# Kernel optimization log

Hardware: AMD Instinct MI355X
Metric: run time of the kernel (lower is better)

Reference implementation:

```python
import jax, jax.numpy as jnp
import numpy as np

S, B, K = 1024, 16, 1024
QD, KD = 1024, 1024


def setup_inputs() -> dict:
    key = jax.random.key(0)
    k1, k2, k3, k4 = jax.random.split(key, 4)
    queries = jax.random.normal(k1, (S, B, QD), dtype=jnp.float32)
    keys = jax.random.normal(k2, (B, K, KD), dtype=jnp.float32)
    null_mask = jax.random.randint(k3, (B, K), 0, 2).astype(jnp.bool_)
    W_in = jax.random.normal(k4, (KD, QD), dtype=jnp.float32) * 0.02
    return {"queries": queries, "keys": keys, "null_mask": null_mask, "W_in": W_in}


def reference(queries, keys, null_mask, W_in):
    # queries: (S, B, QD); keys: (B, K, KD); null_mask: (B, K); W_in: (KD, QD)
    t_query = jnp.einsum('sbq,dq->sbd', queries, W_in)          # linear_in, no bias
    alpha = jnp.einsum('sbd,bkd->sbk', t_query, keys)           # unscaled bilinear scores
    alpha = jnp.where(null_mask[None, :, :], -jnp.inf, alpha)   # masked_fill_
    att_weight = jax.nn.softmax(alpha, axis=2)                  # (S, B, K)
    attened_keys = jnp.einsum('sbk,bkd->sbd', att_weight, keys) # (S, B, KD)
    return (attened_keys, alpha)
```

## Files before the change

kernel.cpp:

```cpp
#include <hip/hip_runtime.h>
#include <math.h>

#define S_DIM 1024
#define B_DIM 16
#define K_DIM 1024
#define QD_DIM 1024
#define KD_DIM 1024
#define MASK_NEG (-3.0e38f)

using short8v = __attribute__((ext_vector_type(8))) short;
using float4v = __attribute__((ext_vector_type(4))) float;
using uint4v  = __attribute__((ext_vector_type(4))) uint;

#define MFMA(a, b, c) __builtin_amdgcn_mfma_f32_16x16x32_bf16(a, b, c, 0, 0, 0)
#define BAR()   __builtin_amdgcn_s_barrier()
#define SB0()   __builtin_amdgcn_sched_barrier(0)
#define PRIO(x) __builtin_amdgcn_s_setprio(x)
#define VMCNT(N) asm volatile("s_waitcnt vmcnt(" #N ")" ::: "memory")
#define LGKM0()  asm volatile("s_waitcnt lgkmcnt(0)" ::: "memory")


__device__ __forceinline__ void gll16(const void* g, void* l) {
    __builtin_amdgcn_global_load_lds((const __attribute__((address_space(1))) unsigned int*)g,
                                     (__attribute__((address_space(3))) unsigned int*)l,
                                     16, 0, 0);
}

__device__ __forceinline__ void split4(const float4 v, uint2& hi, uint2& lo) {
    uint ax = __float_as_uint(v.x), ay = __float_as_uint(v.y);
    uint az = __float_as_uint(v.z), aw = __float_as_uint(v.w);
    hi.x = __builtin_amdgcn_perm(ay, ax, 0x07060302u);
    hi.y = __builtin_amdgcn_perm(aw, az, 0x07060302u);
    float rx = v.x - __uint_as_float(ax & 0xFFFF0000u);
    float ry = v.y - __uint_as_float(ay & 0xFFFF0000u);
    float rz = v.z - __uint_as_float(az & 0xFFFF0000u);
    float rw = v.w - __uint_as_float(aw & 0xFFFF0000u);
    lo.x = __builtin_amdgcn_perm(__float_as_uint(ry), __float_as_uint(rx), 0x07060302u);
    lo.y = __builtin_amdgcn_perm(__float_as_uint(rw), __float_as_uint(rz), 0x07060302u);
}

__device__ __forceinline__ int twiddle(int l) {
    int b0 = (l ^ (l >> 2) ^ (l >> 4)) & 1;
    int b1 = ((l >> 1) ^ (l >> 3)) & 1;
    int b2 = ((l >> 2) ^ (l >> 4)) & 1;
    return (l & 0x38) | (b2 << 2) | (b1 << 1) | b0;
}
__device__ __forceinline__ int fragoff(int R, int quad) {
    return (((R << 2) | quad) ^ (R & 7)) << 3;
}

struct Ctx {
    int w, quad, l15, wm, wn, srow, scol;
    int arow, ac, ws0, ws1;
    int offA[4], offB[8];
};

__device__ __forceinline__ Ctx make_ctx(int t) {
    Ctx c;
    const int lane = t & 63;
    c.w = t >> 6; c.quad = lane >> 4; c.l15 = lane & 15;
    c.wm = c.w >> 1; c.wn = c.w & 1;
    const int sl = twiddle(lane);
    c.srow = c.w * 32 + (sl >> 2);
    c.scol = (sl & 3) * 8;
    c.arow = t >> 1; c.ac = t & 1;
    const int c0 = c.ac * 2;
    c.ws0 = ((c.arow << 2) | c0) ^ (c.arow & 7);
    c.ws1 = ((c.arow << 2) | (c0 + 1)) ^ (c.arow & 7);
    #pragma unroll
    for (int mt = 0; mt < 4; ++mt) { int R = c.wm * 64 + mt * 16 + c.l15; c.offA[mt] = fragoff(R, c.quad); }
    #pragma unroll
    for (int nt = 0; nt < 8; ++nt) { int R = c.wn * 128 + nt * 16 + c.l15; c.offB[nt] = fragoff(R, c.quad); }
    return c;
}

__device__ __forceinline__ void stage2(const short* __restrict__ plane, int row0, int k0,
                                       short* tile, const Ctx& c) {
    const short* g0 = plane + (size_t)(row0 + c.srow) * 1024 + k0 + c.scol;
    gll16(g0, tile + c.w * 1024);
    gll16(g0 + (size_t)16 * 1024, tile + c.w * 1024 + 512);
}

__device__ __forceinline__ void mfma8x4(const short8v (&a)[4], const short8v (&bb)[8],
                                        float4v (&acc)[4][8]) {
    #pragma unroll
    for (int nt = 0; nt < 8; ++nt)
        #pragma unroll
        for (int mt = 0; mt < 4; ++mt)
            acc[mt][nt] = MFMA(a[mt], bb[nt], acc[mt][nt]);
}

__device__ __forceinline__ void load4(const float4* __restrict__ P, int kn, float4 (&v)[4]) {
    #pragma unroll
    for (int i = 0; i < 4; ++i) v[i] = P[kn / 4 + i];
}

__device__ __forceinline__ void write_split(const float4 (&va)[4], short* N0, short* N1,
                                            int ws0, int ws1) {
    uint2 h[4], l[4];
    #pragma unroll
    for (int i = 0; i < 4; ++i) split4(va[i], h[i], l[i]);
    uint4v v0, v1;
    v0[0] = h[0].x; v0[1] = h[0].y; v0[2] = h[1].x; v0[3] = h[1].y;
    v1[0] = h[2].x; v1[1] = h[2].y; v1[2] = h[3].x; v1[3] = h[3].y;
    *(uint4v*)(N0 + ws0 * 8) = v0;
    *(uint4v*)(N0 + ws1 * 8) = v1;
    v0[0] = l[0].x; v0[1] = l[0].y; v0[2] = l[1].x; v0[3] = l[1].y;
    v1[0] = l[2].x; v1[1] = l[2].y; v1[2] = l[3].x; v1[3] = l[3].y;
    *(uint4v*)(N1 + ws0 * 8) = v0;
    *(uint4v*)(N1 + ws1 * 8) = v1;
}

__device__ __forceinline__ void writeA_exp(const float4 (&va)[4], float Mv, float Lv,
                                           short* N0, short* N1, int ws0, int ws1) {
    float4 p[4];
    #pragma unroll
    for (int i = 0; i < 4; ++i) {
        p[i].x = __expf(va[i].x - Mv) * Lv;
        p[i].y = __expf(va[i].y - Mv) * Lv;
        p[i].z = __expf(va[i].z - Mv) * Lv;
        p[i].w = __expf(va[i].w - Mv) * Lv;
    }
    write_split(p, N0, N1, ws0, ws1);
}

__device__ __forceinline__ void loadT(const float* __restrict__ fB, int kn, float4 (&f)[4]) {
    #pragma unroll
    for (int i = 0; i < 4; ++i) f[i] = *(const float4*)(fB + (size_t)(kn + i) * 1024);
}
__device__ __forceinline__ void writeT(const float4 (&f)[4], short* N2, short* N3,
                                       int kq, int dd) {
    #pragma unroll
    for (int e = 0; e < 4; ++e) {
        float4 g;
        g.x = (&f[0].x)[e]; g.y = (&f[1].x)[e];
        g.z = (&f[2].x)[e]; g.w = (&f[3].x)[e];
        uint2 h, l;
        split4(g, h, l);
        const int R = dd * 4 + e;
        const int byteoff = ((((R << 2) | (kq >> 1)) ^ (R & 7)) << 4) + (kq & 1) * 8;
        *(uint2*)((char*)N2 + byteoff) = h;
        *(uint2*)((char*)N3 + byteoff) = l;
    }
}

__global__ __launch_bounds__(256) void k_split(const float* __restrict__ src,
                                               short* __restrict__ h, short* __restrict__ l) {
    const size_t base = ((size_t)blockIdx.x * 256 + threadIdx.x) * 4;
    const float4 v = *(const float4*)(src + base);
    uint2 hh, ll;
    split4(v, hh, ll);
    *(uint2*)(h + base) = hh;
    *(uint2*)(l + base) = ll;
}

__global__ __launch_bounds__(256) void k_stats(const float* __restrict__ alpha,
                                               float* __restrict__ mx,
                                               float* __restrict__ il) {
    const int r = blockIdx.x;
    const int t = threadIdx.x;
    const float4 v = ((const float4*)(alpha + (size_t)r * K_DIM))[t];
    float m = fmaxf(fmaxf(v.x, v.y), fmaxf(v.z, v.w));
    #pragma unroll
    for (int o = 1; o < 64; o <<= 1) m = fmaxf(m, __shfl_xor(m, o, 64));
    __shared__ float redm[4];
    __shared__ float reds[4];
    const int wid = t >> 6;
    if ((t & 63) == 0) redm[wid] = m;
    __syncthreads();
    const float M = fmaxf(fmaxf(redm[0], redm[1]), fmaxf(redm[2], redm[3]));
    float s = expf(v.x - M) + expf(v.y - M) + expf(v.z - M) + expf(v.w - M);
    #pragma unroll
    for (int o = 1; o < 64; o <<= 1) s += __shfl_xor(s, o, 64);
    if ((t & 63) == 0) reds[wid] = s;
    __syncthreads();
    if (t == 0) {
        mx[r] = M;
        il[r] = 1.0f / (reds[0] + reds[1] + reds[2] + reds[3]);
    }
}

template<bool DS>
__device__ __forceinline__ void step_g1(const float4* __restrict__ qP, int kn,
                                        const short* __restrict__ Wh, const short* __restrict__ Wl, int n0,
                                        const short* C0, const short* C1, const short* C2, const short* C3,
                                        short* N0, short* N1, short* N2, short* N3,
                                        const Ctx& c, float4v (&acc)[4][8]) {
    short8v ah[4], bh[8];
    #pragma unroll
    for (int mt = 0; mt < 4; ++mt) ah[mt] = *(const short8v*)(C0 + c.offA[mt]);
    #pragma unroll
    for (int nt = 0; nt < 8; ++nt) bh[nt] = *(const short8v*)(C2 + c.offB[nt]);
    float4 qv[4];
    if (DS) { load4(qP, kn, qv); SB0(); stage2(Wh, n0, kn, N2, c); }
    SB0(); BAR(); LGKM0(); SB0();
    PRIO(1); mfma8x4(ah, bh, acc); PRIO(0); SB0(); BAR();

    short8v al[4];
    #pragma unroll
    for (int mt = 0; mt < 4; ++mt) al[mt] = *(const short8v*)(C1 + c.offA[mt]);
    if (DS) { stage2(Wl, n0, kn, N3, c); }
    SB0(); BAR(); LGKM0(); SB0();
    PRIO(1); mfma8x4(al, bh, acc); PRIO(0); SB0(); BAR();

    if (DS) { VMCNT(4); } else { VMCNT(0); }
    SB0(); BAR();
    short8v bl[8];
    #pragma unroll
    for (int nt = 0; nt < 8; ++nt) bl[nt] = *(const short8v*)(C3 + c.offB[nt]);
    LGKM0(); SB0();
    PRIO(1); mfma8x4(ah, bl, acc); PRIO(0);
    if (DS) {
        write_split(qv, N0, N1, c.ws0, c.ws1);
        LGKM0();
        VMCNT(2);
    }
    SB0(); BAR();
}

__global__ __launch_bounds__(512, 2) void g1k(const float* __restrict__ Q,
                                              const short* __restrict__ Wh, const short* __restrict__ Wl,
                                              short* __restrict__ TQh, short* __restrict__ TQl) {
    __shared__ __align__(16) short lds[65536];
    const int t = threadIdx.x;
    const int m0 = blockIdx.y * 256, n0 = blockIdx.x * 256;
    const Ctx c = make_ctx(t);
    const float4* qP = (const float4*)(Q + (size_t)(m0 + c.arow) * QD_DIM + c.ac * 16);
    short *T00 = lds,         *T01 = lds + 8192,  *T02 = lds + 16384, *T03 = lds + 24576;
    short *T10 = lds + 32768, *T11 = lds + 40960, *T12 = lds + 49152, *T13 = lds + 57344;

    float4v acc[4][8] = {};
    {
        float4 qv[4];
        load4(qP, 0, qv); SB0();
        stage2(Wh, n0, 0, T02, c);
        stage2(Wl, n0, 0, T03, c);
        VMCNT(4); SB0();
        write_split(qv, T00, T01, c.ws0, c.ws1);
        LGKM0();
        VMCNT(2); SB0();
        BAR();
    }
    #pragma unroll 1
    for (int it = 0; it < 15; ++it) {
        step_g1<true>(qP, (2 * it + 1) * 32, Wh, Wl, n0, T00, T01, T02, T03, T10, T11, T12, T13, c, acc);
        step_g1<true>(qP, (2 * it + 2) * 32, Wh, Wl, n0, T10, T11, T12, T13, T00, T01, T02, T03, c, acc);
    }
    step_g1<true >(qP, 31 * 32, Wh, Wl, n0, T00, T01, T02, T03, T10, T11, T12, T13, c, acc);
    step_g1<false>(qP, 0,       Wh, Wl, n0, T10, T11, T12, T13, T00, T01, T02, T03, c, acc);

    #pragma unroll
    for (int mt = 0; mt < 4; ++mt)
        #pragma unroll
        for (int reg = 0; reg < 4; ++reg) {
            const int m = m0 + c.wm * 64 + mt * 16 + c.quad * 4 + reg;
            const int s = m >> 4, bq = m & 15;
            short* th = TQh + (size_t)bq * 1048576 + (size_t)s * 1024;
            short* tl = TQl + (size_t)bq * 1048576 + (size_t)s * 1024;
            #pragma unroll
            for (int nt = 0; nt < 8; ++nt) {
                const int n = n0 + c.wn * 128 + nt * 16 + c.l15;
                const float x = acc[mt][nt][reg];
                const uint u = __float_as_uint(x);
                th[n] = (short)(u >> 16);
                const float r2 = x - __uint_as_float(u & 0xFFFF0000u);
                tl[n] = (short)(__float_as_uint(r2) >> 16);
            }
        }
}

template<bool DS>
__device__ __forceinline__ void step_g2(const float4* __restrict__ kP, int kn,
                                        const short* __restrict__ Ahp, const short* __restrict__ Alp, int m0,
                                        const short* C0, const short* C1, const short* C2, const short* C3,
                                        short* N0, short* N1, short* N2, short* N3,
                                        const Ctx& c, float4v (&acc)[4][8]) {
    short8v ah[4], bh[8];
    #pragma unroll
    for (int mt = 0; mt < 4; ++mt) ah[mt] = *(const short8v*)(C0 + c.offA[mt]);
    #pragma unroll
    for (int nt = 0; nt < 8; ++nt) bh[nt] = *(const short8v*)(C2 + c.offB[nt]);
    float4 kv[4];
    if (DS) { load4(kP, kn, kv); SB0(); stage2(Ahp, m0, kn, N0, c); VMCNT(6); }
    else    { VMCNT(0); }
    SB0(); BAR(); LGKM0(); SB0();
    PRIO(1); mfma8x4(ah, bh, acc); PRIO(0); SB0(); BAR();

    short8v al[4];
    #pragma unroll
    for (int mt = 0; mt < 4; ++mt) al[mt] = *(const short8v*)(C1 + c.offA[mt]);
    if (DS) { stage2(Alp, m0, kn, N1, c); }
    SB0(); BAR(); LGKM0(); SB0();
    PRIO(1); mfma8x4(al, bh, acc); PRIO(0); SB0(); BAR();

    if (DS) { VMCNT(4); } else { VMCNT(0); }
    SB0(); BAR();
    short8v bl[8];
    #pragma unroll
    for (int nt = 0; nt < 8; ++nt) bl[nt] = *(const short8v*)(C3 + c.offB[nt]);
    LGKM0(); SB0();
    PRIO(1); mfma8x4(ah, bl, acc); PRIO(0);
    if (DS) {
        write_split(kv, N2, N3, c.ws0, c.ws1);
        LGKM0();
        VMCNT(2);
    }
    SB0(); BAR();
}

__global__ __launch_bounds__(512, 2) void g2k(const short* __restrict__ TQh, const short* __restrict__ TQl,
                                              const float* __restrict__ keys,
                                              const int* __restrict__ mask, float* __restrict__ alpha) {
    __shared__ __align__(16) short lds[65536];
    const int t = threadIdx.x;
    const int m0 = blockIdx.y * 256, n0 = blockIdx.x * 256, b = blockIdx.z;
    const Ctx c = make_ctx(t);
    const short* Ahp = TQh + (size_t)b * 1048576;
    const short* Alp = TQl + (size_t)b * 1048576;
    const float* Kb = keys + (size_t)b * K_DIM * KD_DIM;
    const float4* kP = (const float4*)(Kb + (size_t)(n0 + c.arow) * KD_DIM + c.ac * 16);
    short *T00 = lds,         *T01 = lds + 8192,  *T02 = lds + 16384, *T03 = lds + 24576;
    short *T10 = lds + 32768, *T11 = lds + 40960, *T12 = lds + 49152, *T13 = lds + 57344;

    float4v acc[4][8] = {};
    {
        float4 kv[4];
        load4(kP, 0, kv); SB0();
        stage2(Ahp, m0, 0, T00, c);
        VMCNT(2); SB0();
        write_split(kv, T02, T03, c.ws0, c.ws1);
        LGKM0(); SB0();
        stage2(Alp, m0, 0, T01, c);
        VMCNT(2); SB0();
        BAR();
    }
    #pragma unroll 1
    for (int it = 0; it < 15; ++it) {
        step_g2<true>(kP, (2 * it + 1) * 32, Ahp, Alp, m0, T00, T01, T02, T03, T10, T11, T12, T13, c, acc);
        step_g2<true>(kP, (2 * it + 2) * 32, Ahp, Alp, m0, T10, T11, T12, T13, T00, T01, T02, T03, c, acc);
    }
    step_g2<true >(kP, 31 * 32, Ahp, Alp, m0, T00, T01, T02, T03, T10, T11, T12, T13, c, acc);
    step_g2<false>(kP, 0,       Ahp, Alp, m0, T10, T11, T12, T13, T00, T01, T02, T03, c, acc);

    int mk[8];
    #pragma unroll
    for (int nt = 0; nt < 8; ++nt)
        mk[nt] = mask[b * K_DIM + n0 + c.wn * 128 + nt * 16 + c.l15];
    #pragma unroll
    for (int mt = 0; mt < 4; ++mt)
        #pragma unroll
        for (int reg = 0; reg < 4; ++reg) {
            const int m = m0 + c.wm * 64 + mt * 16 + c.quad * 4 + reg;
            #pragma unroll
            for (int nt = 0; nt < 8; ++nt) {
                const int n = n0 + c.wn * 128 + nt * 16 + c.l15;
                alpha[((size_t)m * B_DIM + b) * K_DIM + n] = mk[nt] ? MASK_NEG : acc[mt][nt][reg];
            }
        }
}

template<bool DS>
__device__ __forceinline__ void step_g3(const float4* __restrict__ aP, const float* __restrict__ fB, int kn,
                                        const short* C0, const short* C1, const short* C2, const short* C3,
                                        short* N0, short* N1, short* N2, short* N3,
                                        const Ctx& c, float Mv, float Lv, int kq, int dd,
                                        float4v (&acc)[4][8]) {
    short8v ah[4], bh[8];
    #pragma unroll
    for (int mt = 0; mt < 4; ++mt) ah[mt] = *(const short8v*)(C0 + c.offA[mt]);
    #pragma unroll
    for (int nt = 0; nt < 8; ++nt) bh[nt] = *(const short8v*)(C2 + c.offB[nt]);
    float4 av[4];
    if (DS) { load4(aP, kn, av); }
    SB0(); BAR(); LGKM0(); SB0();
    PRIO(1); mfma8x4(ah, bh, acc); PRIO(0); SB0(); BAR();

    short8v al[4];
    #pragma unroll
    for (int mt = 0; mt < 4; ++mt) al[mt] = *(const short8v*)(C1 + c.offA[mt]);
    float4 f[4];
    if (DS) { loadT(fB, kn, f); }
    SB0(); BAR(); LGKM0(); SB0();
    PRIO(1); mfma8x4(al, bh, acc); PRIO(0); SB0(); BAR();

    VMCNT(0);
    SB0(); BAR();
    short8v bl[8];
    #pragma unroll
    for (int nt = 0; nt < 8; ++nt) bl[nt] = *(const short8v*)(C3 + c.offB[nt]);
    LGKM0(); SB0();
    PRIO(1); mfma8x4(ah, bl, acc); PRIO(0);
    if (DS) {
        writeA_exp(av, Mv, Lv, N0, N1, c.ws0, c.ws1);
        writeT(f, N2, N3, kq, dd);
        LGKM0();
    }
    SB0(); BAR();
}

__global__ __launch_bounds__(512, 2) void g3k(const float* __restrict__ alpha,
                                              const float* __restrict__ keys,
                                              const float* __restrict__ mx, const float* __restrict__ il,
                                              float* __restrict__ outk) {
    __shared__ __align__(16) short lds[65536];
    const int t = threadIdx.x;
    const int m0 = blockIdx.y * 256, n0 = blockIdx.x * 256, b = blockIdx.z;
    const Ctx c = make_ctx(t);
    const float* Kb = keys + (size_t)b * K_DIM * KD_DIM;
    const float4* aP = (const float4*)(alpha + ((size_t)(m0 + c.arow) * B_DIM + b) * K_DIM + c.ac * 16);
    const float Mv = mx[(size_t)(m0 + c.arow) * B_DIM + b];
    const float Lv = il[(size_t)(m0 + c.arow) * B_DIM + b];
    const int kq = t & 7, dd = t >> 3;
    const float* fB = Kb + (size_t)(4 * kq) * KD_DIM + n0 + dd * 4;
    short *T00 = lds,         *T01 = lds + 8192,  *T02 = lds + 16384, *T03 = lds + 24576;
    short *T10 = lds + 32768, *T11 = lds + 40960, *T12 = lds + 49152, *T13 = lds + 57344;

    float4v acc[4][8] = {};
    {
        float4 av[4], f[4];
        load4(aP, 0, av); SB0();
        loadT(fB, 0, f);
        VMCNT(0); SB0();
        writeA_exp(av, Mv, Lv, T00, T01, c.ws0, c.ws1);
        writeT(f, T02, T03, kq, dd);
        LGKM0(); SB0();
        BAR();
    }
    #pragma unroll 1
    for (int it = 0; it < 15; ++it) {
        step_g3<true>(aP, fB, (2 * it + 1) * 32, T00, T01, T02, T03, T10, T11, T12, T13, c, Mv, Lv, kq, dd, acc);
        step_g3<true>(aP, fB, (2 * it + 2) * 32, T10, T11, T12, T13, T00, T01, T02, T03, c, Mv, Lv, kq, dd, acc);
    }
    step_g3<true >(aP, fB, 31 * 32, T00, T01, T02, T03, T10, T11, T12, T13, c, Mv, Lv, kq, dd, acc);
    step_g3<false>(aP, fB, 0,       T10, T11, T12, T13, T00, T01, T02, T03, c, Mv, Lv, kq, dd, acc);

    #pragma unroll
    for (int mt = 0; mt < 4; ++mt)
        #pragma unroll
        for (int reg = 0; reg < 4; ++reg) {
            const int m = m0 + c.wm * 64 + mt * 16 + c.quad * 4 + reg;
            #pragma unroll
            for (int nt = 0; nt < 8; ++nt) {
                const int n = n0 + c.wn * 128 + nt * 16 + c.l15;
                outk[((size_t)m * B_DIM + b) * KD_DIM + n] = acc[mt][nt][reg];
            }
        }
}

extern "C" void kernel_launch(void* const* d_in, const int* in_sizes, int n_in,
                              void* d_out, int out_size, void* d_ws, size_t ws_size,
                              hipStream_t stream) {
    const float* Q    = (const float*)d_in[0];
    const float* keys = (const float*)d_in[1];
    const int*   mask = (const int*)d_in[2];
    const float* W    = (const float*)d_in[3];

    float* out_att   = (float*)d_out;
    float* out_alpha = out_att + (size_t)S_DIM * B_DIM * KD_DIM;

    const size_t STREAM = (size_t)B_DIM * 1048576;

    short* TQh = (short*)d_ws;
    short* TQl = TQh + STREAM;
    float* mx  = (float*)((char*)d_ws + ((size_t)64 << 20));
    float* il  = mx + S_DIM * B_DIM;

    short* Wh = (short*)out_att;
    short* Wl = Wh + 1048576;

    dim3 blk(256), blkg(512);

    k_split<<<dim3(1024), blk, 0, stream>>>(W, Wh, Wl);

    g1k<<<dim3(KD_DIM / 256, (S_DIM * B_DIM) / 256), blkg, 0, stream>>>(Q, Wh, Wl, TQh, TQl);

    g2k<<<dim3(K_DIM / 256, S_DIM / 256, B_DIM), blkg, 0, stream>>>(TQh, TQl, keys, mask, out_alpha);

    k_stats<<<dim3(S_DIM * B_DIM), blk, 0, stream>>>(out_alpha, mx, il);

    g3k<<<dim3(KD_DIM / 256, S_DIM / 256, B_DIM), blkg, 0, stream>>>(out_alpha, keys, mx, il, out_att);
}
```

Measured before the change: 596.9 us.

## Pre-split keys into bf16 hi/lo and pre-transpose for GEMM staging

Adds a pass that splits keys into bf16 hi/lo halves once, so g2k can stage both operands with direct global-to-LDS loads instead of loading fp32 keys into registers and splitting them per tile. Adds a transpose-and-split kernel that writes keys^T as hi/lo into workspace, reusing the TQ buffer once g2k is done, so g3k also stages B via global-to-LDS and only converts the softmax A operand in registers. This removes repeated per-block conversion and the strided transpose loads in g3k. The cost is extra full passes over keys (split plus transpose) and scratch space borrowed from the output buffers.

Result: faster. 553.2 us (-7.3%).

```diff
diff --git a/kernel.cpp b/kernel.cpp
--- a/kernel.cpp
+++ b/kernel.cpp
@@ -124,26 +124,6 @@
     write_split(p, N0, N1, ws0, ws1);
 }
 
-__device__ __forceinline__ void loadT(const float* __restrict__ fB, int kn, float4 (&f)[4]) {
-    #pragma unroll
-    for (int i = 0; i < 4; ++i) f[i] = *(const float4*)(fB + (size_t)(kn + i) * 1024);
-}
-__device__ __forceinline__ void writeT(const float4 (&f)[4], short* N2, short* N3,
-                                       int kq, int dd) {
-    #pragma unroll
-    for (int e = 0; e < 4; ++e) {
-        float4 g;
-        g.x = (&f[0].x)[e]; g.y = (&f[1].x)[e];
-        g.z = (&f[2].x)[e]; g.w = (&f[3].x)[e];
-        uint2 h, l;
-        split4(g, h, l);
-        const int R = dd * 4 + e;
-        const int byteoff = ((((R << 2) | (kq >> 1)) ^ (R & 7)) << 4) + (kq & 1) * 8;
-        *(uint2*)((char*)N2 + byteoff) = h;
-        *(uint2*)((char*)N3 + byteoff) = l;
-    }
-}
-
 __global__ __launch_bounds__(256) void k_split(const float* __restrict__ src,
                                                short* __restrict__ h, short* __restrict__ l) {
     const size_t base = ((size_t)blockIdx.x * 256 + threadIdx.x) * 4;
@@ -152,6 +132,25 @@
     split4(v, hh, ll);
     *(uint2*)(h + base) = hh;
     *(uint2*)(l + base) = ll;
+}
+
+__global__ __launch_bounds__(256) void k_transpose(const float* __restrict__ keys,
+                                                   short* __restrict__ th, short* __restrict__ tl) {
+    __shared__ float T[32][33];
+    const int t = threadIdx.x;
+    const int b = blockIdx.z, d0 = blockIdx.x * 32, k0 = blockIdx.y * 32;
+    const float* Kb = keys + (size_t)b * K_DIM * KD_DIM;
+    const int ry = t >> 3, cx = (t & 7) * 4;
+    const float4 v = *(const float4*)(Kb + (size_t)(k0 + ry) * KD_DIM + d0 + cx);
+    T[ry][cx] = v.x; T[ry][cx + 1] = v.y; T[ry][cx + 2] = v.z; T[ry][cx + 3] = v.w;
+    __syncthreads();
+    float4 g;
+    g.x = T[cx][ry]; g.y = T[cx + 1][ry]; g.z = T[cx + 2][ry]; g.w = T[cx + 3][ry];
+    uint2 hh, ll;
+    split4(g, hh, ll);
+    const size_t o = (size_t)b * K_DIM * KD_DIM + (size_t)(d0 + ry) * K_DIM + k0 + cx;
+    *(uint2*)(th + o) = hh;
+    *(uint2*)(tl + o) = ll;
 }
 
 __global__ __launch_bounds__(256) void k_stats(const float* __restrict__ alpha,
@@ -270,8 +269,9 @@
 }
 
 template<bool DS>
-__device__ __forceinline__ void step_g2(const float4* __restrict__ kP, int kn,
-                                        const short* __restrict__ Ahp, const short* __restrict__ Alp, int m0,
+__device__ __forceinline__ void step_gg(const short* __restrict__ Ahp, const short* __restrict__ Alp,
+                                        const short* __restrict__ Bhp, const short* __restrict__ Blp,
+                                        int m0, int n0, int kn,
                                         const short* C0, const short* C1, const short* C2, const short* C3,
                                         short* N0, short* N1, short* N2, short* N3,
                                         const Ctx& c, float4v (&acc)[4][8]) {
@@ -280,8 +280,7 @@
     for (int mt = 0; mt < 4; ++mt) ah[mt] = *(const short8v*)(C0 + c.offA[mt]);
     #pragma unroll
     for (int nt = 0; nt < 8; ++nt) bh[nt] = *(const short8v*)(C2 + c.offB[nt]);
-    float4 kv[4];
-    if (DS) { load4(kP, kn, kv); SB0(); stage2(Ahp, m0, kn, N0, c); VMCNT(6); }
+    if (DS) { stage2(Ahp, m0, kn, N0, c); stage2(Bhp, n0, kn, N2, c); VMCNT(4); }
     else    { VMCNT(0); }
     SB0(); BAR(); LGKM0(); SB0();
     PRIO(1); mfma8x4(ah, bh, acc); PRIO(0); SB0(); BAR();
@@ -289,59 +288,45 @@
     short8v al[4];
     #pragma unroll
     for (int mt = 0; mt < 4; ++mt) al[mt] = *(const short8v*)(C1 + c.offA[mt]);
-    if (DS) { stage2(Alp, m0, kn, N1, c); }
+    if (DS) { stage2(Alp, m0, kn, N1, c); stage2(Blp, n0, kn, N3, c); }
     SB0(); BAR(); LGKM0(); SB0();
     PRIO(1); mfma8x4(al, bh, acc); PRIO(0); SB0(); BAR();
 
-    if (DS) { VMCNT(4); } else { VMCNT(0); }
-    SB0(); BAR();
     short8v bl[8];
     #pragma unroll
     for (int nt = 0; nt < 8; ++nt) bl[nt] = *(const short8v*)(C3 + c.offB[nt]);
-    LGKM0(); SB0();
-    PRIO(1); mfma8x4(ah, bl, acc); PRIO(0);
-    if (DS) {
-        write_split(kv, N2, N3, c.ws0, c.ws1);
-        LGKM0();
-        VMCNT(2);
-    }
-    SB0(); BAR();
+    if (DS) { VMCNT(4); }
+    SB0(); BAR(); LGKM0(); SB0();
+    PRIO(1); mfma8x4(ah, bl, acc); PRIO(0); SB0(); BAR();
+}
+
+__device__ __forceinline__ void core_gg(const short* __restrict__ Ahp, const short* __restrict__ Alp,
+                                        const short* __restrict__ Bhp, const short* __restrict__ Blp,
+                                        int m0, int n0, short* lds, const Ctx& c, float4v (&acc)[4][8]) {
+    short *T00 = lds,         *T01 = lds + 8192,  *T02 = lds + 16384, *T03 = lds + 24576;
+    short *T10 = lds + 32768, *T11 = lds + 40960, *T12 = lds + 49152, *T13 = lds + 57344;
+    stage2(Ahp, m0, 0, T00, c); stage2(Bhp, n0, 0, T02, c);
+    stage2(Alp, m0, 0, T01, c); stage2(Blp, n0, 0, T03, c);
+    VMCNT(4); SB0(); BAR();
+    #pragma unroll 1
+    for (int it = 0; it < 15; ++it) {
+        step_gg<true>(Ahp, Alp, Bhp, Blp, m0, n0, (2 * it + 1) * 32, T00, T01, T02, T03, T10, T11, T12, T13, c, acc);
+        step_gg<true>(Ahp, Alp, Bhp, Blp, m0, n0, (2 * it + 2) * 32, T10, T11, T12, T13, T00, T01, T02, T03, c, acc);
+    }
+    step_gg<true >(Ahp, Alp, Bhp, Blp, m0, n0, 31 * 32, T00, T01, T02, T03, T10, T11, T12, T13, c, acc);
+    step_gg<false>(Ahp, Alp, Bhp, Blp, m0, n0, 0,       T10, T11, T12, T13, T00, T01, T02, T03, c, acc);
 }
 
 __global__ __launch_bounds__(512, 2) void g2k(const short* __restrict__ TQh, const short* __restrict__ TQl,
-                                              const float* __restrict__ keys,
+                                              const short* __restrict__ Kh, const short* __restrict__ Kl,
                                               const int* __restrict__ mask, float* __restrict__ alpha) {
     __shared__ __align__(16) short lds[65536];
     const int t = threadIdx.x;
     const int m0 = blockIdx.y * 256, n0 = blockIdx.x * 256, b = blockIdx.z;
     const Ctx c = make_ctx(t);
-    const short* Ahp = TQh + (size_t)b * 1048576;
-    const short* Alp = TQl + (size_t)b * 1048576;
-    const float* Kb = keys + (size_t)b * K_DIM * KD_DIM;
-    const float4* kP = (const float4*)(Kb + (size_t)(n0 + c.arow) * KD_DIM + c.ac * 16);
-    short *T00 = lds,         *T01 = lds + 8192,  *T02 = lds + 16384, *T03 = lds + 24576;
-    short *T10 = lds + 32768, *T11 = lds + 40960, *T12 = lds + 49152, *T13 = lds + 57344;
-
     float4v acc[4][8] = {};
-    {
-        float4 kv[4];
-        load4(kP, 0, kv); SB0();
-        stage2(Ahp, m0, 0, T00, c);
-        VMCNT(2); SB0();
-        write_split(kv, T02, T03, c.ws0, c.ws1);
-        LGKM0(); SB0();
-        stage2(Alp, m0, 0, T01, c);
-        VMCNT(2); SB0();
-        BAR();
-    }
-    #pragma unroll 1
-    for (int it = 0; it < 15; ++it) {
-        step_g2<true>(kP, (2 * it + 1) * 32, Ahp, Alp, m0, T00, T01, T02, T03, T10, T11, T12, T13, c, acc);
-        step_g2<true>(kP, (2 * it + 2) * 32, Ahp, Alp, m0, T10, T11, T12, T13, T00, T01, T02, T03, c, acc);
-    }
-    step_g2<true >(kP, 31 * 32, Ahp, Alp, m0, T00, T01, T02, T03, T10, T11, T12, T13, c, acc);
-    step_g2<false>(kP, 0,       Ahp, Alp, m0, T10, T11, T12, T13, T00, T01, T02, T03, c, acc);
-
+    core_gg(TQh + (size_t)b * 1048576, TQl + (size_t)b * 1048576,
+            Kh + (size_t)b * 1048576, Kl + (size_t)b * 1048576, m0, n0, lds, c, acc);
     int mk[8];
     #pragma unroll
     for (int nt = 0; nt < 8; ++nt)
@@ -360,30 +345,35 @@
 }
 
 template<bool DS>
-__device__ __forceinline__ void step_g3(const float4* __restrict__ aP, const float* __restrict__ fB, int kn,
+__device__ __forceinline__ void step_g3(const float4* __restrict__ aP, int kn,
+                                        const short* __restrict__ Bhp, const short* __restrict__ Blp, int n0,
                                         const short* C0, const short* C1, const short* C2, const short* C3,
                                         short* N0, short* N1, short* N2, short* N3,
-                                        const Ctx& c, float Mv, float Lv, int kq, int dd,
+                                        const Ctx& c, float Mv, float Lv,
                                         float4v (&acc)[4][8]) {
     short8v ah[4], bh[8];
     #pragma unroll
     for (int mt = 0; mt < 4; ++mt) ah[mt] = *(const short8v*)(C0 + c.offA[mt]);
     #pragma unroll
     for (int nt = 0; nt < 8; ++nt) bh[nt] = *(const short8v*)(C2 + c.offB[nt]);
-    float4 av[4];
-    if (DS) { load4(aP, kn, av); }
+    float4 va[4];
+    if (DS) {
+        #pragma unroll
+        for (int i = 0; i < 4; ++i) va[i] = aP[kn / 4 + i];
+        stage2(Bhp, n0, kn, N2, c);
+    }
     SB0(); BAR(); LGKM0(); SB0();
     PRIO(1); mfma8x4(ah, bh, acc); PRIO(0); SB0(); BAR();
 
     short8v al[4];
     #pragma unroll
     for (int mt = 0; mt < 4; ++mt) al[mt] = *(const short8v*)(C1 + c.offA[mt]);
-    float4 f[4];
-    if (DS) { loadT(fB, kn, f); }
+    if (DS) { stage2(Blp, n0, kn, N3, c); }
     SB0(); BAR(); LGKM0(); SB0();
     PRIO(1); mfma8x4(al, bh, acc); PRIO(0); SB0(); BAR();
 
-    VMCNT(0);
+    if (DS) { VMCNT(4); }
+    else    { VMCNT(0); }
     SB0(); BAR();
     short8v bl[8];
     #pragma unroll
@@ -391,48 +381,49 @@
     LGKM0(); SB0();
     PRIO(1); mfma8x4(ah, bl, acc); PRIO(0);
     if (DS) {
-        writeA_exp(av, Mv, Lv, N0, N1, c.ws0, c.ws1);
-        writeT(f, N2, N3, kq, dd);
+        writeA_exp(va, Mv, Lv, N0, N1, c.ws0, c.ws1);
         LGKM0();
+        VMCNT(2);
     }
     SB0(); BAR();
 }
 
 __global__ __launch_bounds__(512, 2) void g3k(const float* __restrict__ alpha,
-                                              const float* __restrict__ keys,
+                                              const short* __restrict__ KTh, const short* __restrict__ KTl,
                                               const float* __restrict__ mx, const float* __restrict__ il,
                                               float* __restrict__ outk) {
     __shared__ __align__(16) short lds[65536];
     const int t = threadIdx.x;
     const int m0 = blockIdx.y * 256, n0 = blockIdx.x * 256, b = blockIdx.z;
     const Ctx c = make_ctx(t);
-    const float* Kb = keys + (size_t)b * K_DIM * KD_DIM;
+    const short* Bhp = KTh + (size_t)b * 1048576;
+    const short* Blp = KTl + (size_t)b * 1048576;
     const float4* aP = (const float4*)(alpha + ((size_t)(m0 + c.arow) * B_DIM + b) * K_DIM + c.ac * 16);
     const float Mv = mx[(size_t)(m0 + c.arow) * B_DIM + b];
     const float Lv = il[(size_t)(m0 + c.arow) * B_DIM + b];
-    const int kq = t & 7, dd = t >> 3;
-    const float* fB = Kb + (size_t)(4 * kq) * KD_DIM + n0 + dd * 4;
     short *T00 = lds,         *T01 = lds + 8192,  *T02 = lds + 16384, *T03 = lds + 24576;
     short *T10 = lds + 32768, *T11 = lds + 40960, *T12 = lds + 49152, *T13 = lds + 57344;
 
     float4v acc[4][8] = {};
     {
-        float4 av[4], f[4];
-        load4(aP, 0, av); SB0();
-        loadT(fB, 0, f);
-        VMCNT(0); SB0();
-        writeA_exp(av, Mv, Lv, T00, T01, c.ws0, c.ws1);
-        writeT(f, T02, T03, kq, dd);
-        LGKM0(); SB0();
-        BAR();
+        float4 va[4];
+        #pragma unroll
+        for (int i = 0; i < 4; ++i) va[i] = aP[i];
+        stage2(Bhp, n0, 0, T02, c);
+        stage2(Blp, n0, 0, T03, c);
+        VMCNT(4);
+        writeA_exp(va, Mv, Lv, T00, T01, c.ws0, c.ws1);
+        LGKM0();
+        VMCNT(2);
+        SB0(); BAR();
     }
     #pragma unroll 1
     for (int it = 0; it < 15; ++it) {
-        step_g3<true>(aP, fB, (2 * it + 1) * 32, T00, T01, T02, T03, T10, T11, T12, T13, c, Mv, Lv, kq, dd, acc);
-        step_g3<true>(aP, fB, (2 * it + 2) * 32, T10, T11, T12, T13, T00, T01, T02, T03, c, Mv, Lv, kq, dd, acc);
-    }
-    step_g3<true >(aP, fB, 31 * 32, T00, T01, T02, T03, T10, T11, T12, T13, c, Mv, Lv, kq, dd, acc);
-    step_g3<false>(aP, fB, 0,       T10, T11, T12, T13, T00, T01, T02, T03, c, Mv, Lv, kq, dd, acc);
+        step_g3<true>(aP, (2 * it + 1) * 32, Bhp, Blp, n0, T00, T01, T02, T03, T10, T11, T12, T13, c, Mv, Lv, acc);
+        step_g3<true>(aP, (2 * it + 2) * 32, Bhp, Blp, n0, T10, T11, T12, T13, T00, T01, T02, T03, c, Mv, Lv, acc);
+    }
+    step_g3<true >(aP, 31 * 32, Bhp, Blp, n0, T00, T01, T02, T03, T10, T11, T12, T13, c, Mv, Lv, acc);
+    step_g3<false>(aP, 0,       Bhp, Blp, n0, T10, T11, T12, T13, T00, T01, T02, T03, c, Mv, Lv, acc);
 
     #pragma unroll
     for (int mt = 0; mt < 4; ++mt)
@@ -462,21 +453,28 @@
 
     short* TQh = (short*)d_ws;
     short* TQl = TQh + STREAM;
+    short* KTh = (short*)d_ws;
+    short* KTl = KTh + STREAM;
     float* mx  = (float*)((char*)d_ws + ((size_t)64 << 20));
     float* il  = mx + S_DIM * B_DIM;
 
-    short* Wh = (short*)out_att;
-    short* Wl = Wh + 1048576;
+    short* Wh  = (short*)out_alpha;
+    short* Wl  = Wh + 1048576;
+    short* Khs = (short*)out_att;
+    short* Kls = Khs + STREAM;
 
     dim3 blk(256), blkg(512);
 
     k_split<<<dim3(1024), blk, 0, stream>>>(W, Wh, Wl);
+    k_split<<<dim3(16384), blk, 0, stream>>>(keys, Khs, Kls);
 
     g1k<<<dim3(KD_DIM / 256, (S_DIM * B_DIM) / 256), blkg, 0, stream>>>(Q, Wh, Wl, TQh, TQl);
 
-    g2k<<<dim3(K_DIM / 256, S_DIM / 256, B_DIM), blkg, 0, stream>>>(TQh, TQl, keys, mask, out_alpha);
+    g2k<<<dim3(K_DIM / 256, S_DIM / 256, B_DIM), blkg, 0, stream>>>(TQh, TQl, Khs, Kls, mask, out_alpha);
+
+    k_transpose<<<dim3(32, 32, B_DIM), blk, 0, stream>>>(keys, KTh, KTl);
 
     k_stats<<<dim3(S_DIM * B_DIM), blk, 0, stream>>>(out_alpha, mx, il);
 
-    g3k<<<dim3(KD_DIM / 256, S_DIM / 256, B_DIM), blkg, 0, stream>>>(out_alpha, keys, mx, il, out_att);
-}
+    g3k<<<dim3(KD_DIM / 256, S_DIM / 256, B_DIM), blkg, 0, stream>>>(out_alpha, KTh, KTl, mx, il, out_att);
+}
```
